# Kernel tuning notes

Hardware: AMD Instinct MI355X
Metric: run time of the kernel (lower is better)

## Reference

```python
import jax, jax.numpy as jnp
import numpy as np

N = 100000
E = 1600000
D_IN = 128
D_H = 128
BN_EPS = 1e-5


def setup_inputs() -> dict:
    key = jax.random.key(0)
    ks = jax.random.split(key, 8)
    x = jax.random.normal(ks[0], (N, D_IN), dtype=jnp.float32)
    edge_index = jax.random.randint(ks[1], (2, E), 0, N, dtype=jnp.int64)
    # MLP params (Linear stores weight as [out, in])
    lim1 = 1.0 / np.sqrt(D_IN)
    W1 = jax.random.uniform(ks[2], (D_H, D_IN), minval=-lim1, maxval=lim1, dtype=jnp.float32)
    b1 = jax.random.uniform(ks[3], (D_H,), minval=-lim1, maxval=lim1, dtype=jnp.float32)
    gamma = jnp.ones((D_H,), dtype=jnp.float32)
    beta = jnp.zeros((D_H,), dtype=jnp.float32)
    lim2 = 1.0 / np.sqrt(D_H)
    W2 = jax.random.uniform(ks[4], (D_H, D_H), minval=-lim2, maxval=lim2, dtype=jnp.float32)
    b2 = jax.random.uniform(ks[5], (D_H,), minval=-lim2, maxval=lim2, dtype=jnp.float32)
    eps = jnp.float32(0.0)  # trainable eps parameter, init 0
    return {"x": x, "edge_index": edge_index, "eps": eps, "W1": W1, "b1": b1,
            "gamma": gamma, "beta": beta, "W2": W2, "b2": b2}


def reference(x, edge_index, eps, W1, b1, gamma, beta, W2, b2):
    src = edge_index[0]
    dst = edge_index[1]
    # Augmented edges = original + reversed + self-loops.
    # aggr[dst] += x[src]; aggr[src] += x[dst]; aggr[i] += x[i]
    aggr = jnp.zeros_like(x).at[dst].add(x[src]).at[src].add(x[dst]) + x
    h = (1.0 + eps) * x + aggr              # [N, D_IN]
    h = h @ W1.T + b1                        # [N, D_H]
    # BatchNorm1d in training mode: batch stats, biased variance
    mean = jnp.mean(h, axis=0)
    var = jnp.mean(jnp.square(h - mean), axis=0)
    h = gamma * (h - mean) * jax.lax.rsqrt(var + BN_EPS) + beta
    h = jax.nn.relu(h)
    return h @ W2.T + b2                     # [N, D_H]
```

## Files before the change

### kernel.cpp

```cpp
#include <hip/hip_runtime.h>
#include <hip/hip_fp16.h>

#define N_NODES 100000
#define EDGES   1600000
#define D       128
#define BN_EPS  1e-5f
#define TM      64
#define NT      ((N_NODES + TM - 1) / TM)
#define GGRID   782
#define NB      ((N_NODES + 255) >> 8)
#define SLOT    9216
#define L1E     8
#define L1TILE  (256 * L1E)

typedef __attribute__((ext_vector_type(8))) short short8;
typedef __attribute__((ext_vector_type(4))) float f32x4;

__device__ __forceinline__ unsigned short bf_hi(float f) {
    unsigned u = __float_as_uint(f);
    unsigned t = u + 0x7FFF + ((u >> 16) & 1);
    return (unsigned short)(t >> 16);
}
__device__ __forceinline__ float bf_val(unsigned short h) {
    return __uint_as_float(((unsigned)h) << 16);
}

__global__ void convert_zero(const float* __restrict__ x, __half* __restrict__ xh,
                             int* __restrict__ zbase,
                             const float* __restrict__ W1, const float* __restrict__ W2,
                             unsigned short* __restrict__ w1h, unsigned short* __restrict__ w1l,
                             unsigned short* __restrict__ w2h, unsigned short* __restrict__ w2l) {
    int gid = blockIdx.x * blockDim.x + threadIdx.x;
    if (gid < 2560) zbase[gid] = 0;
    if (gid < 16384) {
        float f = W1[gid];
        unsigned short h = bf_hi(f);
        w1h[gid] = h;
        w1l[gid] = bf_hi(f - bf_val(h));
    } else if (gid < 32768) {
        int j = gid - 16384;
        float f = W2[j];
        unsigned short h = bf_hi(f);
        w2h[j] = h;
        w2l[j] = bf_hi(f - bf_val(h));
    }
    const int n4 = N_NODES * (D / 4);
    if (gid < n4) {
        float4 v = ((const float4*)x)[gid];
        __half2 h0 = __float22half2_rn(make_float2(v.x, v.y));
        __half2 h1 = __float22half2_rn(make_float2(v.z, v.w));
        ((__half2*)xh)[(long long)gid * 2 + 0] = h0;
        ((__half2*)xh)[(long long)gid * 2 + 1] = h1;
    }
}

__launch_bounds__(256)
__global__ void partition_pairs(const int* __restrict__ ei, int* __restrict__ gcur,
                                int* __restrict__ pairs) {
    __shared__ int cnt[NB];
    __shared__ int cbase[NB];
    const int tid = threadIdx.x;
    for (int i = tid; i < NB; i += 256) cnt[i] = 0;
    __syncthreads();

    int bbA[L1E], rrA[L1E], pkA[L1E];
    int bbB[L1E], rrB[L1E], pkB[L1E];
    const int t0 = blockIdx.x * L1TILE + tid;
#pragma unroll
    for (int j = 0; j < L1E; ++j) {
        int t = t0 + j * 256;
        bbA[j] = -1;
        bbB[j] = -1;
        if (t < EDGES) {
            int s = ei[t];
            int d = ei[EDGES + t];
            bbA[j] = d >> 8;
            pkA[j] = ((d & 255) << 17) | s;
            rrA[j] = atomicAdd(&cnt[bbA[j]], 1);
            bbB[j] = s >> 8;
            pkB[j] = ((s & 255) << 17) | d;
            rrB[j] = atomicAdd(&cnt[bbB[j]], 1);
        }
    }
    __syncthreads();
    for (int i = tid; i < NB; i += 256) {
        int c = cnt[i];
        cbase[i] = c ? (i * SLOT + atomicAdd(&gcur[i], c)) : 0;
    }
    __syncthreads();
#pragma unroll
    for (int j = 0; j < L1E; ++j) {
        if (bbA[j] >= 0) {
            pairs[cbase[bbA[j]] + rrA[j]] = pkA[j];
            pairs[cbase[bbB[j]] + rrB[j]] = pkB[j];
        }
    }
}

__launch_bounds__(256)
__global__ void bucket_fill(int* __restrict__ pairs, const int* __restrict__ gcur,
                            int* __restrict__ ofs, int* __restrict__ oen) {
    __shared__ int sP[SLOT];
    __shared__ int lc[256];
    __shared__ int cur[256];
    const int b    = blockIdx.x;
    const int tid  = threadIdx.x;
    const int base = b * SLOT;
    const int m    = min(gcur[b], SLOT);
    for (int i = tid; i < m; i += 256) sP[i] = pairs[base + i];
    lc[tid] = 0;
    __syncthreads();
    for (int i = tid; i < m; i += 256) atomicAdd(&lc[sP[i] >> 17], 1);
    __syncthreads();
    int v = lc[tid];
    for (int d = 1; d < 256; d <<= 1) {
        int u = (tid >= d) ? lc[tid - d] : 0;
        __syncthreads();
        lc[tid] += u;
        __syncthreads();
    }
    int abs0 = base + lc[tid] - v;
    cur[tid] = abs0;
    const int n = (b << 8) + tid;
    if (n < N_NODES) { ofs[n] = abs0; oen[n] = abs0 + v; }
    __syncthreads();
    for (int i = tid; i < m; i += 256) {
        int p = sP[i];
        int r = atomicAdd(&cur[p >> 17], 1);
        pairs[r] = p & 0x1FFFF;
    }
}

__launch_bounds__(256)
__global__ void gather_aggr(const __half* __restrict__ xh,
                            const int* __restrict__ adj, const int* __restrict__ ofs,
                            const int* __restrict__ oen, const float* __restrict__ eps_p,
                            unsigned int* __restrict__ hh, unsigned int* __restrict__ hl,
                            int nbase) {
    int node = nbase + blockIdx.x * 4 + (threadIdx.x >> 6);
    if (node >= N_NODES) return;
    int lane = threadIdx.x & 63;
    int b = ofs[node];
    int e = oen[node];
    const __half2* xp = (const __half2*)xh;
    float ax = 0.f, ay = 0.f;
    int i = b;
    for (; i + 8 <= e; i += 8) {
        int n0 = adj[i],     n1 = adj[i + 1], n2 = adj[i + 2], n3 = adj[i + 3];
        int n4 = adj[i + 4], n5 = adj[i + 5], n6 = adj[i + 6], n7 = adj[i + 7];
        __half2 v0 = xp[(unsigned)n0 * 64u + lane];
        __half2 v1 = xp[(unsigned)n1 * 64u + lane];
        __half2 v2 = xp[(unsigned)n2 * 64u + lane];
        __half2 v3 = xp[(unsigned)n3 * 64u + lane];
        __half2 v4 = xp[(unsigned)n4 * 64u + lane];
        __half2 v5 = xp[(unsigned)n5 * 64u + lane];
        __half2 v6 = xp[(unsigned)n6 * 64u + lane];
        __half2 v7 = xp[(unsigned)n7 * 64u + lane];
        float2 f0 = __half22float2(v0);
        float2 f1 = __half22float2(v1);
        float2 f2 = __half22float2(v2);
        float2 f3 = __half22float2(v3);
        float2 f4 = __half22float2(v4);
        float2 f5 = __half22float2(v5);
        float2 f6 = __half22float2(v6);
        float2 f7 = __half22float2(v7);
        ax += ((f0.x + f1.x) + (f2.x + f3.x)) + ((f4.x + f5.x) + (f6.x + f7.x));
        ay += ((f0.y + f1.y) + (f2.y + f3.y)) + ((f4.y + f5.y) + (f6.y + f7.y));
    }
    for (; i + 4 <= e; i += 4) {
        int n0 = adj[i], n1 = adj[i + 1], n2 = adj[i + 2], n3 = adj[i + 3];
        __half2 v0 = xp[(unsigned)n0 * 64u + lane];
        __half2 v1 = xp[(unsigned)n1 * 64u + lane];
        __half2 v2 = xp[(unsigned)n2 * 64u + lane];
        __half2 v3 = xp[(unsigned)n3 * 64u + lane];
        float2 f0 = __half22float2(v0);
        float2 f1 = __half22float2(v1);
        float2 f2 = __half22float2(v2);
        float2 f3 = __half22float2(v3);
        ax += (f0.x + f1.x) + (f2.x + f3.x);
        ay += (f0.y + f1.y) + (f2.y + f3.y);
    }
    for (; i < e; ++i) {
        __half2 v = xp[(unsigned)adj[i] * 64u + lane];
        float2 f = __half22float2(v);
        ax += f.x;
        ay += f.y;
    }
    float2 xs = __half22float2(xp[(unsigned)node * 64u + lane]);
    float sc = 2.0f + eps_p[0];
    float ox = fmaf(sc, xs.x, ax);
    float oy = fmaf(sc, xs.y, ay);
    unsigned short hx = bf_hi(ox), hy = bf_hi(oy);
    unsigned short lx = bf_hi(ox - bf_val(hx)), ly = bf_hi(oy - bf_val(hy));
    hh[(long long)node * 64 + lane] = (unsigned)hx | ((unsigned)hy << 16);
    hl[(long long)node * 64 + lane] = (unsigned)lx | ((unsigned)ly << 16);
}

__launch_bounds__(256)
__global__ void gemm1_mfma(const unsigned short* __restrict__ hh,
                           const unsigned short* __restrict__ hl,
                           const unsigned short* __restrict__ w1h,
                           const unsigned short* __restrict__ w1l,
                           const float* __restrict__ b1, float* __restrict__ h1,
                           float* __restrict__ stats) {
    __shared__ unsigned short sH[TM][136];
    __shared__ unsigned short sL[TM][136];
    const int tid = threadIdx.x;
    const int wv  = tid >> 6;
    const int ln  = tid & 63;
    const int lc  = ln & 15;
    const int qd  = ln >> 4;
    const int sr  = tid >> 4;
    const int sc8 = tid & 15;

    short8 Bh[4][2], Bl[4][2];
#pragma unroll
    for (int kk = 0; kk < 4; ++kk)
#pragma unroll
        for (int tl = 0; tl < 2; ++tl) {
            int woff = (wv * 32 + tl * 16 + lc) * D + kk * 32 + qd * 8;
            Bh[kk][tl] = *(const short8*)(w1h + woff);
            Bl[kk][tl] = *(const short8*)(w1l + woff);
        }
    float bb[2];
    bb[0] = b1[wv * 32 + lc];
    bb[1] = b1[wv * 32 + 16 + lc];

    float sAcc[2] = {0.f, 0.f}, qAcc[2] = {0.f, 0.f};

    uint4 vh[4], vl[4];
    int tile = blockIdx.x;
#pragma unroll
    for (int i = 0; i < 4; ++i) {
        int gr = tile * TM + sr + i * 16;
        vh[i] = make_uint4(0, 0, 0, 0);
        vl[i] = make_uint4(0, 0, 0, 0);
        if (gr < N_NODES) {
            vh[i] = *(const uint4*)(hh + (long long)gr * D + sc8 * 8);
            vl[i] = *(const uint4*)(hl + (long long)gr * D + sc8 * 8);
        }
    }

    while (tile < NT) {
#pragma unroll
        for (int i = 0; i < 4; ++i) {
            *(uint4*)&sH[sr + i * 16][sc8 * 8] = vh[i];
            *(uint4*)&sL[sr + i * 16][sc8 * 8] = vl[i];
        }
        __syncthreads();
        int nxt = tile + GGRID;
        if (nxt < NT) {
#pragma unroll
            for (int i = 0; i < 4; ++i) {
                int gr = nxt * TM + sr + i * 16;
                vh[i] = make_uint4(0, 0, 0, 0);
                vl[i] = make_uint4(0, 0, 0, 0);
                if (gr < N_NODES) {
                    vh[i] = *(const uint4*)(hh + (long long)gr * D + sc8 * 8);
                    vl[i] = *(const uint4*)(hl + (long long)gr * D + sc8 * 8);
                }
            }
        }

        f32x4 acc[4][2];
#pragma unroll
        for (int m = 0; m < 4; ++m)
#pragma unroll
            for (int tl = 0; tl < 2; ++tl) acc[m][tl] = (f32x4){0.f, 0.f, 0.f, 0.f};

#pragma unroll
        for (int kk = 0; kk < 4; ++kk) {
#pragma unroll
            for (int m = 0; m < 4; ++m) {
                short8 ah = *(const short8*)&sH[m * 16 + lc][kk * 32 + qd * 8];
                short8 al = *(const short8*)&sL[m * 16 + lc][kk * 32 + qd * 8];
#pragma unroll
                for (int tl = 0; tl < 2; ++tl) {
                    acc[m][tl] = __builtin_amdgcn_mfma_f32_16x16x32_bf16(ah, Bh[kk][tl], acc[m][tl], 0, 0, 0);
                    acc[m][tl] = __builtin_amdgcn_mfma_f32_16x16x32_bf16(al, Bh[kk][tl], acc[m][tl], 0, 0, 0);
                    acc[m][tl] = __builtin_amdgcn_mfma_f32_16x16x32_bf16(ah, Bl[kk][tl], acc[m][tl], 0, 0, 0);
                }
            }
        }

        const int row0 = tile * TM;
#pragma unroll
        for (int m = 0; m < 4; ++m)
#pragma unroll
            for (int tl = 0; tl < 2; ++tl) {
                int col = wv * 32 + tl * 16 + lc;
#pragma unroll
                for (int r = 0; r < 4; ++r) {
                    int grow = row0 + m * 16 + qd * 4 + r;
                    if (grow < N_NODES) {
                        float o = acc[m][tl][r] + bb[tl];
                        h1[(long long)grow * D + col] = o;
                        sAcc[tl] += o;
                        qAcc[tl] += o * o;
                    }
                }
            }
        __syncthreads();
        tile = nxt;
    }

    const int rep = blockIdx.x & 7;
#pragma unroll
    for (int tl = 0; tl < 2; ++tl) {
        float s = sAcc[tl], q = qAcc[tl];
        s += __shfl_xor(s, 16); s += __shfl_xor(s, 32);
        q += __shfl_xor(q, 16); q += __shfl_xor(q, 32);
        if (qd == 0) {
            int col = wv * 32 + tl * 16 + lc;
            atomicAdd(&stats[rep * 256 + col], s);
            atomicAdd(&stats[rep * 256 + 128 + col], q);
        }
    }
}

__launch_bounds__(256)
__global__ void gemm2_mfma(float* __restrict__ h1out,
                           const unsigned short* __restrict__ w2h,
                           const unsigned short* __restrict__ w2l,
                           const float* __restrict__ b2, const float* __restrict__ stats,
                           const float* __restrict__ gamma, const float* __restrict__ beta) {
    __shared__ unsigned short sH[TM][136];
    __shared__ unsigned short sL[TM][136];
    __shared__ float sScale[128];
    __shared__ float sShift[128];
    const int tid = threadIdx.x;
    const int wv  = tid >> 6;
    const int ln  = tid & 63;
    const int lc  = ln & 15;
    const int qd  = ln >> 4;
    const int sr  = tid >> 5;
    const int sc4 = tid & 31;

    if (tid < 128) {
        float s = 0.f, q = 0.f;
#pragma unroll
        for (int r = 0; r < 8; ++r) {
            s += stats[r * 256 + tid];
            q += stats[r * 256 + 128 + tid];
        }
        float mean = s * (1.0f / N_NODES);
        float var  = fmaxf(q * (1.0f / N_NODES) - mean * mean, 0.0f);
        float sc   = gamma[tid] * rsqrtf(var + BN_EPS);
        sScale[tid] = sc;
        sShift[tid] = beta[tid] - mean * sc;
    }

    short8 Bh[4][2], Bl[4][2];
#pragma unroll
    for (int kk = 0; kk < 4; ++kk)
#pragma unroll
        for (int tl = 0; tl < 2; ++tl) {
            int woff = (wv * 32 + tl * 16 + lc) * D + kk * 32 + qd * 8;
            Bh[kk][tl] = *(const short8*)(w2h + woff);
            Bl[kk][tl] = *(const short8*)(w2l + woff);
        }
    float bb[2];
    bb[0] = b2[wv * 32 + lc];
    bb[1] = b2[wv * 32 + 16 + lc];

    __syncthreads();

    float4 pf[8];
    int tile = blockIdx.x;
#pragma unroll
    for (int i = 0; i < 8; ++i) {
        int gr = tile * TM + sr + i * 8;
        pf[i] = make_float4(0.f, 0.f, 0.f, 0.f);
        if (gr < N_NODES)
            pf[i] = *(const float4*)(h1out + (long long)gr * D + sc4 * 4);
    }

    while (tile < NT) {
        float4 scv = *(const float4*)&sScale[sc4 * 4];
        float4 shv = *(const float4*)&sShift[sc4 * 4];
#pragma unroll
        for (int i = 0; i < 8; ++i) {
            int gr = tile * TM + sr + i * 8;
            float4 v = pf[i];
            if (gr < N_NODES) {
                v.x = fmaxf(0.f, fmaf(v.x, scv.x, shv.x));
                v.y = fmaxf(0.f, fmaf(v.y, scv.y, shv.y));
                v.z = fmaxf(0.f, fmaf(v.z, scv.z, shv.z));
                v.w = fmaxf(0.f, fmaf(v.w, scv.w, shv.w));
            } else {
                v = make_float4(0.f, 0.f, 0.f, 0.f);
            }
            unsigned short h0 = bf_hi(v.x), h1b = bf_hi(v.y), h2 = bf_hi(v.z), h3 = bf_hi(v.w);
            unsigned short l0 = bf_hi(v.x - bf_val(h0)), l1 = bf_hi(v.y - bf_val(h1b));
            unsigned short l2 = bf_hi(v.z - bf_val(h2)), l3 = bf_hi(v.w - bf_val(h3));
            int r = sr + i * 8;
            *(uint2*)&sH[r][sc4 * 4] = make_uint2((unsigned)h0 | ((unsigned)h1b << 16),
                                                  (unsigned)h2 | ((unsigned)h3 << 16));
            *(uint2*)&sL[r][sc4 * 4] = make_uint2((unsigned)l0 | ((unsigned)l1 << 16),
                                                  (unsigned)l2 | ((unsigned)l3 << 16));
        }
        __syncthreads();
        int nxt = tile + GGRID;
        if (nxt < NT) {
#pragma unroll
            for (int i = 0; i < 8; ++i) {
                int gr = nxt * TM + sr + i * 8;
                pf[i] = make_float4(0.f, 0.f, 0.f, 0.f);
                if (gr < N_NODES)
                    pf[i] = *(const float4*)(h1out + (long long)gr * D + sc4 * 4);
            }
        }

        f32x4 acc[4][2];
#pragma unroll
        for (int m = 0; m < 4; ++m)
#pragma unroll
            for (int tl = 0; tl < 2; ++tl) acc[m][tl] = (f32x4){0.f, 0.f, 0.f, 0.f};

#pragma unroll
        for (int kk = 0; kk < 4; ++kk) {
#pragma unroll
            for (int m = 0; m < 4; ++m) {
                short8 ah = *(const short8*)&sH[m * 16 + lc][kk * 32 + qd * 8];
                short8 al = *(const short8*)&sL[m * 16 + lc][kk * 32 + qd * 8];
#pragma unroll
                for (int tl = 0; tl < 2; ++tl) {
                    acc[m][tl] = __builtin_amdgcn_mfma_f32_16x16x32_bf16(ah, Bh[kk][tl], acc[m][tl], 0, 0, 0);
                    acc[m][tl] = __builtin_amdgcn_mfma_f32_16x16x32_bf16(al, Bh[kk][tl], acc[m][tl], 0, 0, 0);
                    acc[m][tl] = __builtin_amdgcn_mfma_f32_16x16x32_bf16(ah, Bl[kk][tl], acc[m][tl], 0, 0, 0);
                }
            }
        }

        const int row0 = tile * TM;
#pragma unroll
        for (int m = 0; m < 4; ++m)
#pragma unroll
            for (int tl = 0; tl < 2; ++tl) {
                int col = wv * 32 + tl * 16 + lc;
#pragma unroll
                for (int r = 0; r < 4; ++r) {
                    int grow = row0 + m * 16 + qd * 4 + r;
                    if (grow < N_NODES)
                        h1out[(long long)grow * D + col] = acc[m][tl][r] + bb[tl];
                }
            }
        __syncthreads();
        tile = nxt;
    }
}

extern "C" void kernel_launch(void* const* d_in, const int* in_sizes, int n_in,
                              void* d_out, int out_size, void* d_ws, size_t ws_size,
                              hipStream_t stream) {
    const float* x     = (const float*)d_in[0];
    const int*   ei    = (const int*)d_in[1];
    const float* eps_p = (const float*)d_in[2];
    const float* W1    = (const float*)d_in[3];
    const float* b1    = (const float*)d_in[4];
    const float* gamma = (const float*)d_in[5];
    const float* beta  = (const float*)d_in[6];
    const float* W2    = (const float*)d_in[7];
    const float* b2    = (const float*)d_in[8];

    unsigned int* hh  = (unsigned int*)d_ws;
    unsigned int* hl  = hh + (long long)N_NODES * 64;
    float* stats = (float*)(hl + (long long)N_NODES * 64);
    int*   gcur  = (int*)(stats + 2048);
    int*   ofs   = gcur + 512;
    int*   oen   = ofs + N_NODES;
    unsigned short* w1h = (unsigned short*)(oen + N_NODES);
    unsigned short* w1l = w1h + 16384;
    unsigned short* w2h = w1l + 16384;
    unsigned short* w2l = w2h + 16384;

    float* out   = (float*)d_out;
    __half* xh   = (__half*)d_out;
    int*  pairs  = (int*)((char*)d_out + (size_t)N_NODES * 256);
    int*  adj    = pairs;

    {
        int grid = (N_NODES * (D / 4) + 255) / 256;
        convert_zero<<<grid, 256, 0, stream>>>(x, xh, (int*)stats,
                                               W1, W2, w1h, w1l, w2h, w2l);
    }
    {
        int grid = (EDGES + L1TILE - 1) / L1TILE;
        partition_pairs<<<grid, 256, 0, stream>>>(ei, gcur, pairs);
    }
    {
        bucket_fill<<<NB, 256, 0, stream>>>(pairs, gcur, ofs, oen);
    }
    {
        int half = N_NODES / 2;
        int grid = (half + 3) / 4;
        gather_aggr<<<grid, 256, 0, stream>>>(xh, adj, ofs, oen, eps_p, hh, hl, 0);
        int grid2 = (N_NODES - half + 3) / 4;
        gather_aggr<<<grid2, 256, 0, stream>>>(xh, adj, ofs, oen, eps_p, hh, hl, half);
    }
    {
        gemm1_mfma<<<GGRID, 256, 0, stream>>>((const unsigned short*)hh, (const unsigned short*)hl,
                                              w1h, w1l, b1, out, stats);
    }
    {
        gemm2_mfma<<<GGRID, 256, 0, stream>>>(out, w2h, w2l, b2, stats, gamma, beta);
    }
}
```

Measured before the change: 355.1 us.

## Apply W1 before aggregation and fuse bias and BN stats into gather

Uses linearity to compute x@W1^T first, storing the result as fp16, and then gathers and aggregates these projected rows. The bias add and the BatchNorm sum and sum-of-squares accumulation move into a persistent grid-stride gather kernel, which reduces them per block in shared memory and spreads atomics over 32 replicas. This removes the separate x-to-half conversion pass and the hi/lo bf16 intermediate writes and reads between gather and GEMM1. In exchange, the intermediate is rounded to fp16 after the matmul, which changes numerical error.

```diff
diff --git a/kernel.cpp b/kernel.cpp
--- a/kernel.cpp
+++ b/kernel.cpp
@@ -12,6 +12,9 @@
 #define SLOT    9216
 #define L1E     8
 #define L1TILE  (256 * L1E)
+#define GBLKS   1536
+#define GWAVES  (GBLKS * 4)
+#define NREP    32
 
 typedef __attribute__((ext_vector_type(8))) short short8;
 typedef __attribute__((ext_vector_type(4))) float f32x4;
@@ -25,32 +28,23 @@
     return __uint_as_float(((unsigned)h) << 16);
 }
 
-__global__ void convert_zero(const float* __restrict__ x, __half* __restrict__ xh,
-                             int* __restrict__ zbase,
-                             const float* __restrict__ W1, const float* __restrict__ W2,
-                             unsigned short* __restrict__ w1h, unsigned short* __restrict__ w1l,
-                             unsigned short* __restrict__ w2h, unsigned short* __restrict__ w2l) {
+__global__ void zero_split(int* __restrict__ zbase,
+                           const float* __restrict__ W1, const float* __restrict__ W2,
+                           unsigned short* __restrict__ w1h, unsigned short* __restrict__ w1l,
+                           unsigned short* __restrict__ w2h, unsigned short* __restrict__ w2l) {
     int gid = blockIdx.x * blockDim.x + threadIdx.x;
-    if (gid < 2560) zbase[gid] = 0;
+    if (gid < 8704) zbase[gid] = 0;
     if (gid < 16384) {
         float f = W1[gid];
         unsigned short h = bf_hi(f);
         w1h[gid] = h;
         w1l[gid] = bf_hi(f - bf_val(h));
-    } else if (gid < 32768) {
+    } else {
         int j = gid - 16384;
         float f = W2[j];
         unsigned short h = bf_hi(f);
         w2h[j] = h;
         w2l[j] = bf_hi(f - bf_val(h));
-    }
-    const int n4 = N_NODES * (D / 4);
-    if (gid < n4) {
-        float4 v = ((const float4*)x)[gid];
-        __half2 h0 = __float22half2_rn(make_float2(v.x, v.y));
-        __half2 h1 = __float22half2_rn(make_float2(v.z, v.w));
-        ((__half2*)xh)[(long long)gid * 2 + 0] = h0;
-        ((__half2*)xh)[(long long)gid * 2 + 1] = h1;
     }
 }
 
@@ -132,77 +126,10 @@
 }
 
 __launch_bounds__(256)
-__global__ void gather_aggr(const __half* __restrict__ xh,
-                            const int* __restrict__ adj, const int* __restrict__ ofs,
-                            const int* __restrict__ oen, const float* __restrict__ eps_p,
-                            unsigned int* __restrict__ hh, unsigned int* __restrict__ hl,
-                            int nbase) {
-    int node = nbase + blockIdx.x * 4 + (threadIdx.x >> 6);
-    if (node >= N_NODES) return;
-    int lane = threadIdx.x & 63;
-    int b = ofs[node];
-    int e = oen[node];
-    const __half2* xp = (const __half2*)xh;
-    float ax = 0.f, ay = 0.f;
-    int i = b;
-    for (; i + 8 <= e; i += 8) {
-        int n0 = adj[i],     n1 = adj[i + 1], n2 = adj[i + 2], n3 = adj[i + 3];
-        int n4 = adj[i + 4], n5 = adj[i + 5], n6 = adj[i + 6], n7 = adj[i + 7];
-        __half2 v0 = xp[(unsigned)n0 * 64u + lane];
-        __half2 v1 = xp[(unsigned)n1 * 64u + lane];
-        __half2 v2 = xp[(unsigned)n2 * 64u + lane];
-        __half2 v3 = xp[(unsigned)n3 * 64u + lane];
-        __half2 v4 = xp[(unsigned)n4 * 64u + lane];
-        __half2 v5 = xp[(unsigned)n5 * 64u + lane];
-        __half2 v6 = xp[(unsigned)n6 * 64u + lane];
-        __half2 v7 = xp[(unsigned)n7 * 64u + lane];
-        float2 f0 = __half22float2(v0);
-        float2 f1 = __half22float2(v1);
-        float2 f2 = __half22float2(v2);
-        float2 f3 = __half22float2(v3);
-        float2 f4 = __half22float2(v4);
-        float2 f5 = __half22float2(v5);
-        float2 f6 = __half22float2(v6);
-        float2 f7 = __half22float2(v7);
-        ax += ((f0.x + f1.x) + (f2.x + f3.x)) + ((f4.x + f5.x) + (f6.x + f7.x));
-        ay += ((f0.y + f1.y) + (f2.y + f3.y)) + ((f4.y + f5.y) + (f6.y + f7.y));
-    }
-    for (; i + 4 <= e; i += 4) {
-        int n0 = adj[i], n1 = adj[i + 1], n2 = adj[i + 2], n3 = adj[i + 3];
-        __half2 v0 = xp[(unsigned)n0 * 64u + lane];
-        __half2 v1 = xp[(unsigned)n1 * 64u + lane];
-        __half2 v2 = xp[(unsigned)n2 * 64u + lane];
-        __half2 v3 = xp[(unsigned)n3 * 64u + lane];
-        float2 f0 = __half22float2(v0);
-        float2 f1 = __half22float2(v1);
-        float2 f2 = __half22float2(v2);
-        float2 f3 = __half22float2(v3);
-        ax += (f0.x + f1.x) + (f2.x + f3.x);
-        ay += (f0.y + f1.y) + (f2.y + f3.y);
-    }
-    for (; i < e; ++i) {
-        __half2 v = xp[(unsigned)adj[i] * 64u + lane];
-        float2 f = __half22float2(v);
-        ax += f.x;
-        ay += f.y;
-    }
-    float2 xs = __half22float2(xp[(unsigned)node * 64u + lane]);
-    float sc = 2.0f + eps_p[0];
-    float ox = fmaf(sc, xs.x, ax);
-    float oy = fmaf(sc, xs.y, ay);
-    unsigned short hx = bf_hi(ox), hy = bf_hi(oy);
-    unsigned short lx = bf_hi(ox - bf_val(hx)), ly = bf_hi(oy - bf_val(hy));
-    hh[(long long)node * 64 + lane] = (unsigned)hx | ((unsigned)hy << 16);
-    hl[(long long)node * 64 + lane] = (unsigned)lx | ((unsigned)ly << 16);
-}
-
-__launch_bounds__(256)
-__global__ void gemm1_mfma(const unsigned short* __restrict__ hh,
-                           const unsigned short* __restrict__ hl,
+__global__ void gemm0_mfma(const float* __restrict__ x,
                            const unsigned short* __restrict__ w1h,
                            const unsigned short* __restrict__ w1l,
-                           const float* __restrict__ b1, float* __restrict__ h1,
-                           float* __restrict__ stats) {
+                           __half* __restrict__ yh) {
     __shared__ unsigned short sH[TM][136];
     __shared__ unsigned short sL[TM][136];
     const int tid = threadIdx.x;
@@ -210,8 +137,8 @@
     const int ln  = tid & 63;
     const int lc  = ln & 15;
     const int qd  = ln >> 4;
-    const int sr  = tid >> 4;
-    const int sc8 = tid & 15;
+    const int sr  = tid >> 5;
+    const int sc4 = tid & 31;
 
     short8 Bh[4][2], Bl[4][2];
 #pragma unroll
@@ -222,43 +149,39 @@
             Bh[kk][tl] = *(const short8*)(w1h + woff);
             Bl[kk][tl] = *(const short8*)(w1l + woff);
         }
-    float bb[2];
-    bb[0] = b1[wv * 32 + lc];
-    bb[1] = b1[wv * 32 + 16 + lc];
-
-    float sAcc[2] = {0.f, 0.f}, qAcc[2] = {0.f, 0.f};
-
-    uint4 vh[4], vl[4];
+
+    float4 pf[8];
     int tile = blockIdx.x;
 #pragma unroll
-    for (int i = 0; i < 4; ++i) {
-        int gr = tile * TM + sr + i * 16;
-        vh[i] = make_uint4(0, 0, 0, 0);
-        vl[i] = make_uint4(0, 0, 0, 0);
-        if (gr < N_NODES) {
-            vh[i] = *(const uint4*)(hh + (long long)gr * D + sc8 * 8);
-            vl[i] = *(const uint4*)(hl + (long long)gr * D + sc8 * 8);
-        }
+    for (int i = 0; i < 8; ++i) {
+        int gr = tile * TM + sr + i * 8;
+        pf[i] = make_float4(0.f, 0.f, 0.f, 0.f);
+        if (gr < N_NODES)
+            pf[i] = *(const float4*)(x + (long long)gr * D + sc4 * 4);
     }
 
     while (tile < NT) {
 #pragma unroll
-        for (int i = 0; i < 4; ++i) {
-            *(uint4*)&sH[sr + i * 16][sc8 * 8] = vh[i];
-            *(uint4*)&sL[sr + i * 16][sc8 * 8] = vl[i];
+        for (int i = 0; i < 8; ++i) {
+            float4 v = pf[i];
+            unsigned short h0 = bf_hi(v.x), h1b = bf_hi(v.y), h2 = bf_hi(v.z), h3 = bf_hi(v.w);
+            unsigned short l0 = bf_hi(v.x - bf_val(h0)), l1 = bf_hi(v.y - bf_val(h1b));
+            unsigned short l2 = bf_hi(v.z - bf_val(h2)), l3 = bf_hi(v.w - bf_val(h3));
+            int r = sr + i * 8;
+            *(uint2*)&sH[r][sc4 * 4] = make_uint2((unsigned)h0 | ((unsigned)h1b << 16),
+                                                  (unsigned)h2 | ((unsigned)h3 << 16));
+            *(uint2*)&sL[r][sc4 * 4] = make_uint2((unsigned)l0 | ((unsigned)l1 << 16),
+                                                  (unsigned)l2 | ((unsigned)l3 << 16));
         }
         __syncthreads();
         int nxt = tile + GGRID;
         if (nxt < NT) {
 #pragma unroll
-            for (int i = 0; i < 4; ++i) {
-                int gr = nxt * TM + sr + i * 16;
-                vh[i] = make_uint4(0, 0, 0, 0);
-                vl[i] = make_uint4(0, 0, 0, 0);
-                if (gr < N_NODES) {
-                    vh[i] = *(const uint4*)(hh + (long long)gr * D + sc8 * 8);
-                    vl[i] = *(const uint4*)(hl + (long long)gr * D + sc8 * 8);
-                }
+            for (int i = 0; i < 8; ++i) {
+                int gr = nxt * TM + sr + i * 8;
+                pf[i] = make_float4(0.f, 0.f, 0.f, 0.f);
+                if (gr < N_NODES)
+                    pf[i] = *(const float4*)(x + (long long)gr * D + sc4 * 4);
             }
         }
 
@@ -292,29 +215,97 @@
 #pragma unroll
                 for (int r = 0; r < 4; ++r) {
                     int grow = row0 + m * 16 + qd * 4 + r;
-                    if (grow < N_NODES) {
-                        float o = acc[m][tl][r] + bb[tl];
-                        h1[(long long)grow * D + col] = o;
-                        sAcc[tl] += o;
-                        qAcc[tl] += o * o;
-                    }
+                    if (grow < N_NODES)
+                        yh[(long long)grow * D + col] = __float2half(acc[m][tl][r]);
                 }
             }
         __syncthreads();
         tile = nxt;
     }
-
-    const int rep = blockIdx.x & 7;
-#pragma unroll
-    for (int tl = 0; tl < 2; ++tl) {
-        float s = sAcc[tl], q = qAcc[tl];
-        s += __shfl_xor(s, 16); s += __shfl_xor(s, 32);
-        q += __shfl_xor(q, 16); q += __shfl_xor(q, 32);
-        if (qd == 0) {
-            int col = wv * 32 + tl * 16 + lc;
-            atomicAdd(&stats[rep * 256 + col], s);
-            atomicAdd(&stats[rep * 256 + 128 + col], q);
-        }
+}
+
+__launch_bounds__(256)
+__global__ void gather_aggr(const __half* __restrict__ yh,
+                            const int* __restrict__ adj, const int* __restrict__ ofs,
+                            const int* __restrict__ oen, const float* __restrict__ eps_p,
+                            const float* __restrict__ b1,
+                            float* __restrict__ h1, float* __restrict__ stats) {
+    const int wv   = threadIdx.x >> 6;
+    const int lane = threadIdx.x & 63;
+    const int wave = blockIdx.x * 4 + wv;
+    const __half2* xp = (const __half2*)yh;
+    const float sc = 2.0f + eps_p[0];
+    const float2 b1c = ((const float2*)b1)[lane];
+    float sx = 0.f, sy = 0.f, qx = 0.f, qy = 0.f;
+
+    for (int node = wave; node < N_NODES; node += GWAVES) {
+        int b = ofs[node];
+        int e = oen[node];
+        float ax = 0.f, ay = 0.f;
+        int i = b;
+        for (; i + 8 <= e; i += 8) {
+            int n0 = adj[i],     n1 = adj[i + 1], n2 = adj[i + 2], n3 = adj[i + 3];
+            int n4 = adj[i + 4], n5 = adj[i + 5], n6 = adj[i + 6], n7 = adj[i + 7];
+            __half2 v0 = xp[(unsigned)n0 * 64u + lane];
+            __half2 v1 = xp[(unsigned)n1 * 64u + lane];
+            __half2 v2 = xp[(unsigned)n2 * 64u + lane];
+            __half2 v3 = xp[(unsigned)n3 * 64u + lane];
+            __half2 v4 = xp[(unsigned)n4 * 64u + lane];
+            __half2 v5 = xp[(unsigned)n5 * 64u + lane];
+            __half2 v6 = xp[(unsigned)n6 * 64u + lane];
+            __half2 v7 = xp[(unsigned)n7 * 64u + lane];
+            float2 f0 = __half22float2(v0);
+            float2 f1 = __half22float2(v1);
+            float2 f2 = __half22float2(v2);
+            float2 f3 = __half22float2(v3);
+            float2 f4 = __half22float2(v4);
+            float2 f5 = __half22float2(v5);
+            float2 f6 = __half22float2(v6);
+            float2 f7 = __half22float2(v7);
+            ax += ((f0.x + f1.x) + (f2.x + f3.x)) + ((f4.x + f5.x) + (f6.x + f7.x));
+            ay += ((f0.y + f1.y) + (f2.y + f3.y)) + ((f4.y + f5.y) + (f6.y + f7.y));
+        }
+        for (; i + 4 <= e; i += 4) {
+            int n0 = adj[i], n1 = adj[i + 1], n2 = adj[i + 2], n3 = adj[i + 3];
+            __half2 v0 = xp[(unsigned)n0 * 64u + lane];
+            __half2 v1 = xp[(unsigned)n1 * 64u + lane];
+            __half2 v2 = xp[(unsigned)n2 * 64u + lane];
+            __half2 v3 = xp[(unsigned)n3 * 64u + lane];
+            float2 f0 = __half22float2(v0);
+            float2 f1 = __half22float2(v1);
+            float2 f2 = __half22float2(v2);
+            float2 f3 = __half22float2(v3);
+            ax += (f0.x + f1.x) + (f2.x + f3.x);
+            ay += (f0.y + f1.y) + (f2.y + f3.y);
+        }
+        for (; i < e; ++i) {
+            __half2 v = xp[(unsigned)adj[i] * 64u + lane];
+            float2 f = __half22float2(v);
+            ax += f.x;
+            ay += f.y;
+        }
+        float2 ys = __half22float2(xp[(unsigned)node * 64u + lane]);
+        float ox = fmaf(sc, ys.x, ax) + b1c.x;
+        float oy = fmaf(sc, ys.y, ay) + b1c.y;
+        ((float2*)h1)[(long long)node * 64 + lane] = make_float2(ox, oy);
+        sx += ox; sy += oy;
+        qx += ox * ox; qy += oy * oy;
+    }
+
+    __shared__ float4 red[4][64];
+    red[wv][lane] = make_float4(sx, sy, qx, qy);
+    __syncthreads();
+    if (wv == 0) {
+        float4 a = red[0][lane], b4 = red[1][lane], c = red[2][lane], d4 = red[3][lane];
+        float fx = (a.x + b4.x) + (c.x + d4.x);
+        float fy = (a.y + b4.y) + (c.y + d4.y);
+        float gx = (a.z + b4.z) + (c.z + d4.z);
+        float gy = (a.w + b4.w) + (c.w + d4.w);
+        float* st = stats + (blockIdx.x & (NREP - 1)) * 256;
+        atomicAdd(&st[2 * lane],       fx);
+        atomicAdd(&st[2 * lane + 1],   fy);
+        atomicAdd(&st[128 + 2 * lane],     gx);
+        atomicAdd(&st[128 + 2 * lane + 1], gy);
     }
 }
 
@@ -339,7 +330,7 @@
     if (tid < 128) {
         float s = 0.f, q = 0.f;
 #pragma unroll
-        for (int r = 0; r < 8; ++r) {
+        for (int r = 0; r < NREP; ++r) {
             s += stats[r * 256 + tid];
             q += stats[r * 256 + 128 + tid];
         }
@@ -463,26 +454,22 @@
     const float* W2    = (const float*)d_in[7];
     const float* b2    = (const float*)d_in[8];
 
-    unsigned int* hh  = (unsigned int*)d_ws;
-    unsigned int* hl  = hh + (long long)N_NODES * 64;
-    float* stats = (float*)(hl + (long long)N_NODES * 64);
-    int*   gcur  = (int*)(stats + 2048);
-    int*   ofs   = gcur + 512;
-    int*   oen   = ofs + N_NODES;
+    __half* yh   = (__half*)d_ws;
+    float*  stats = (float*)(yh + (long long)N_NODES * D);
+    int*    gcur  = (int*)(stats + NREP * 256);
+    int*    ofs   = gcur + 512;
+    int*    oen   = ofs + N_NODES;
     unsigned short* w1h = (unsigned short*)(oen + N_NODES);
     unsigned short* w1l = w1h + 16384;
     unsigned short* w2h = w1l + 16384;
     unsigned short* w2l = w2h + 16384;
-
-    float* out   = (float*)d_out;
-    __half* xh   = (__half*)d_out;
-    int*  pairs  = (int*)((char*)d_out + (size_t)N_NODES * 256);
-    int*  adj    = pairs;
-
-    {
-        int grid = (N_NODES * (D / 4) + 255) / 256;
-        convert_zero<<<grid, 256, 0, stream>>>(x, xh, (int*)stats,
-                                               W1, W2, w1h, w1l, w2h, w2l);
+    int*    pairs = (int*)(w2l + 16384);
+    int*    adj   = pairs;
+
+    float* out = (float*)d_out;
+
+    {
+        zero_split<<<128, 256, 0, stream>>>((int*)stats, W1, W2, w1h, w1l, w2h, w2l);
     }
     {
         int grid = (EDGES + L1TILE - 1) / L1TILE;
@@ -492,15 +479,10 @@
         bucket_fill<<<NB, 256, 0, stream>>>(pairs, gcur, ofs, oen);
     }
     {
-        int half = N_NODES / 2;
-        int grid = (half + 3) / 4;
-        gather_aggr<<<grid, 256, 0, stream>>>(xh, adj, ofs, oen, eps_p, hh, hl, 0);
-        int grid2 = (N_NODES - half + 3) / 4;
-        gather_aggr<<<grid2, 256, 0, stream>>>(xh, adj, ofs, oen, eps_p, hh, hl, half);
-    }
-    {
-        gemm1_mfma<<<GGRID, 256, 0, stream>>>((const unsigned short*)hh, (const unsigned short*)hl,
-                                              w1h, w1l, b1, out, stats);
+        gemm0_mfma<<<GGRID, 256, 0, stream>>>(x, w1h, w1l, yh);
+    }
+    {
+        gather_aggr<<<GBLKS, 256, 0, stream>>>(yh, adj, ofs, oen, eps_p, b1, out, stats);
     }
     {
         gemm2_mfma<<<GGRID, 256, 0, stream>>>(out, w2h, w2l, b2, stats, gamma, beta);
```

Result: faster. 345.0 us (-2.8%).
